# Performance work log

Hardware: AMD Instinct MI355X
Metric: run time of the kernel (lower is better)

## Reference

```python
import jax, jax.numpy as jnp
import numpy as np

N_CHARS = 256
EMB = 1024
HID = 2048
SEQ = 4096


def setup_inputs() -> dict:
    key = jax.random.key(0)
    ks = jax.random.split(key, 12)
    s = 0.02
    return {
        "input_seq": jax.random.randint(ks[0], (SEQ,), 0, N_CHARS),
        "hidden": jnp.zeros((HID,), jnp.float32),
        "cell": jnp.zeros((HID,), jnp.float32),
        "emb": jax.random.normal(ks[1], (N_CHARS, EMB), jnp.float32) * s,
        # gate weights stored as [concat, hidden] so step does z @ W + b
        "Wf": jax.random.normal(ks[2], (EMB + HID, HID), jnp.float32) * s,
        "bf": jnp.zeros((HID,), jnp.float32),
        "Wi": jax.random.normal(ks[3], (EMB + HID, HID), jnp.float32) * s,
        "bi": jnp.zeros((HID,), jnp.float32),
        "Wo": jax.random.normal(ks[4], (EMB + HID, HID), jnp.float32) * s,
        "bo": jnp.zeros((HID,), jnp.float32),
        "Wc": jax.random.normal(ks[5], (EMB + HID, HID), jnp.float32) * s,
        "bc": jnp.zeros((HID,), jnp.float32),
        "Wy": jax.random.normal(ks[6], (HID, N_CHARS), jnp.float32) * s,
        "by": jnp.zeros((N_CHARS,), jnp.float32),
    }


def reference(input_seq, hidden, cell, emb, Wf, bf, Wi, bi, Wo, bo, Wc, bc, Wy, by):
    x = emb[input_seq]  # [S, EMB] embedding lookup for whole sequence

    def step(carry, xt):
        h, c = carry
        z = jnp.concatenate([xt, h])           # [EMB+HID]
        f = jax.nn.sigmoid(z @ Wf + bf)        # forget gate
        i = jax.nn.sigmoid(z @ Wi + bi)        # input gate
        g = jnp.tanh(z @ Wc + bc)              # cell candidate
        o = jax.nn.sigmoid(z @ Wo + bo)        # output gate
        c_new = f * c + i * g
        h_new = o * jnp.tanh(c_new)
        y = h_new @ Wy + by                    # [N_CHARS]
        return (h_new, c_new), y

    (h_fin, c_fin), preds = jax.lax.scan(step, (hidden, cell), x)
    return preds, h_fin, c_fin
```

## Files before the change

kernel.cpp:

```cpp
#include <hip/hip_runtime.h>
#include <hip/hip_bf16.h>
#include <stdint.h>

#define NCH  256
#define EMB  1024
#define HID  2048
#define SEQL 4096

static constexpr size_t EG_OFF   = 0;
static constexpr size_t EG_BYTES = (size_t)NCH * 8192 * 4;
static constexpr size_t HS_OFF   = EG_OFF + EG_BYTES;
static constexpr size_t HS_BYTES = (size_t)SEQL * HID * 4;
static constexpr size_t HB_OFF   = HS_OFF + HS_BYTES;
static constexpr size_t HB_BYTES = 2 * HID * 8;
static constexpr size_t CF_OFF   = HB_OFF + HB_BYTES;
static constexpr size_t CF_BYTES = HID * 4;
static constexpr size_t WS_NEED  = CF_OFF + CF_BYTES;

__global__ __launch_bounds__(256) void eg_gemm(
    const float* __restrict__ emb,
    const float* __restrict__ Wf, const float* __restrict__ bf,
    const float* __restrict__ Wi, const float* __restrict__ bi,
    const float* __restrict__ Wo, const float* __restrict__ bo,
    const float* __restrict__ Wc, const float* __restrict__ bc,
    float* __restrict__ Eg)
{
    const int nb  = blockIdx.x & 63;
    const int cb  = blockIdx.x >> 6;
    const int tid = threadIdx.x;
    const int col = tid & 127;
    const int gate = col >> 5;
    const int jj   = col & 31;
    const int j    = nb * 32 + jj;
    const int mh   = tid >> 7;

    __shared__ float embT[32][65];
    __shared__ float Wt[32][128];

    float acc[32];
#pragma unroll
    for (int m = 0; m < 32; ++m) acc[m] = 0.f;

    for (int k0 = 0; k0 < EMB; k0 += 32) {
        __syncthreads();
        for (int i = tid; i < 64 * 32; i += 256) {
            int c = i >> 5, kk = i & 31;
            embT[kk][c] = emb[(size_t)(cb * 64 + c) * EMB + k0 + kk];
        }
        for (int i = tid; i < 32 * 128; i += 256) {
            int kk = i >> 7, cl = i & 127;
            int g2 = cl >> 5;
            int jx = nb * 32 + (cl & 31);
            const float* Wp = (g2 == 0) ? Wf : (g2 == 1) ? Wi : (g2 == 2) ? Wo : Wc;
            Wt[kk][cl] = Wp[(size_t)(k0 + kk) * HID + jx];
        }
        __syncthreads();
#pragma unroll 8
        for (int kk = 0; kk < 32; ++kk) {
            float w = Wt[kk][col];
#pragma unroll
            for (int m = 0; m < 32; ++m)
                acc[m] += embT[kk][mh * 32 + m] * w;
        }
    }
    const float* bias = (gate == 0) ? bf : (gate == 1) ? bi : (gate == 2) ? bo : bc;
    float bv = bias[j];
    for (int m = 0; m < 32; ++m) {
        int c = cb * 64 + mh * 32 + m;
        Eg[(size_t)c * 8192 + (j >> 3) * 32 + gate * 8 + (j & 7)] = acc[m] + bv;
    }
}

__device__ inline void poll2(const void* p0, const void* p1, uint4& a, uint4& b)
{
    asm volatile(
        "global_load_dwordx4 %0, %2, off sc0 sc1\n\t"
        "global_load_dwordx4 %1, %3, off sc0 sc1\n\t"
        "s_waitcnt vmcnt(0)"
        : "=&v"(a), "=&v"(b)
        : "v"(p0), "v"(p1)
        : "memory");
}

#define REP32(M) M(0) M(1) M(2) M(3) M(4) M(5) M(6) M(7) M(8) M(9) M(10) M(11) \
  M(12) M(13) M(14) M(15) M(16) M(17) M(18) M(19) M(20) M(21) M(22) M(23)      \
  M(24) M(25) M(26) M(27) M(28) M(29) M(30) M(31)

__global__ __launch_bounds__(512, 2) void lstm_seq(
    const int*   __restrict__ seq,
    const float* __restrict__ h0,
    const float* __restrict__ c0,
    const float* __restrict__ Wf, const float* __restrict__ Wi,
    const float* __restrict__ Wo, const float* __restrict__ Wc,
    const float* __restrict__ Eg,
    float* __restrict__ Hs,
    unsigned long long* hb2, float* cfin)
{
    const int cu   = blockIdx.x;
    const int tid  = threadIdx.x;
    const int lane = tid & 63;
    const int wave = tid >> 6;
    const int g    = lane >> 4;
    const int kp   = lane & 15;
    const int jcol = cu * 8 + wave;

    const float* W = (g == 0) ? Wf : (g == 1) ? Wi : (g == 2) ? Wo : Wc;

    const float* Wb = W + (size_t)(1024 + kp * 4) * HID + jcol;
#define WDECL(i) float4 w##i;
    REP32(WDECL)
#undef WDECL
#define WLOAD(i) { w##i.x = Wb[(size_t)((i)*64+0)*HID]; \
                   w##i.y = Wb[(size_t)((i)*64+1)*HID]; \
                   w##i.z = Wb[(size_t)((i)*64+2)*HID]; \
                   w##i.w = Wb[(size_t)((i)*64+3)*HID]; \
                   asm volatile("" : "+a"(w##i.x), "+a"(w##i.y), \
                                     "+a"(w##i.z), "+a"(w##i.w)); }
    REP32(WLOAD)
#undef WLOAD

    __shared__ __align__(16) float h_lds[HID];
    __shared__ int seq_lds[SEQL];

    for (int i = tid; i < SEQL; i += 512) seq_lds[i] = seq[i];
    for (int i = tid; i < HID;  i += 512) h_lds[i]   = h0[i];
    float c = 0.f;
    if (lane == 0) c = c0[jcol];
    __syncthreads();

    const float4* hp = (const float4*)h_lds;

    for (int t = 0; t < SEQL; ++t) {
        float egv = Eg[(size_t)seq_lds[t] * 8192 + cu * 32 + g * 8 + wave];

        float accv[4] = {0.f, 0.f, 0.f, 0.f};
#define WMAC(i) { float4 hv = hp[(i)*16 + kp]; \
                  accv[(i)&3] += w##i.x*hv.x + w##i.y*hv.y + w##i.z*hv.z + w##i.w*hv.w; }
        REP32(WMAC)
#undef WMAC
        float sum = (accv[0] + accv[1]) + (accv[2] + accv[3]);

        sum += __shfl_xor(sum, 1, 16);
        sum += __shfl_xor(sum, 2, 16);
        sum += __shfl_xor(sum, 4, 16);
        sum += __shfl_xor(sum, 8, 16);

        float pre = sum + egv;
        float act;
        if (g < 3) {
            act = 1.f / (1.f + __expf(-pre));
        } else {
            float e = __expf(2.f * pre);
            act = 1.f - 2.f / (e + 1.f);
        }
        float i_ = __shfl(act, 16, 64);
        float o_ = __shfl(act, 32, 64);
        float g_ = __shfl(act, 48, 64);

        if (lane == 0) {
            c = act * c + i_ * g_;
            float e2 = __expf(2.f * c);
            float hn = o_ * (1.f - 2.f / (e2 + 1.f));
            Hs[(size_t)t * HID + jcol] = hn;
            unsigned long long pk =
                ((unsigned long long)(unsigned)(t + 1) << 32) |
                (unsigned long long)__float_as_uint(hn);
            __hip_atomic_store(&hb2[(size_t)((t + 1) & 1) * HID + jcol], pk,
                               __ATOMIC_RELAXED, __HIP_MEMORY_SCOPE_AGENT);
        }

        if (t + 1 < SEQL) {
            const unsigned tgt = (unsigned)(t + 1);
            unsigned long long* sl = hb2 + (size_t)((t + 1) & 1) * HID;
            const void* p0 = (const void*)(sl + 4 * tid);
            const void* p1 = (const void*)(sl + 4 * tid + 2);
            uint4 a, b;
            poll2(p0, p1, a, b);
            while (a.y < tgt || a.w < tgt || b.y < tgt || b.w < tgt) {
                __builtin_amdgcn_s_sleep(1);
                poll2(p0, p1, a, b);
            }
            __syncthreads();
            float4 hv;
            hv.x = __uint_as_float(a.x);
            hv.y = __uint_as_float(a.z);
            hv.z = __uint_as_float(b.x);
            hv.w = __uint_as_float(b.z);
            ((float4*)h_lds)[tid] = hv;
            __syncthreads();
        }
    }

    if (lane == 0) cfin[jcol] = c;
}

__global__ __launch_bounds__(256) void y_gemm(
    const float* __restrict__ Hs, const float* __restrict__ Wy,
    const float* __restrict__ by, float* __restrict__ out)
{
    const int rb  = blockIdx.x * 16;
    const int tid = threadIdx.x;
    __shared__ float A[16][68];
    float acc[16];
#pragma unroll
    for (int r = 0; r < 16; ++r) acc[r] = 0.f;

    for (int k0 = 0; k0 < HID; k0 += 64) {
        __syncthreads();
        for (int i = tid; i < 16 * 64; i += 256) {
            int r = i >> 6, kk = i & 63;
            A[r][kk] = Hs[(size_t)(rb + r) * HID + k0 + kk];
        }
        __syncthreads();
#pragma unroll 8
        for (int kk = 0; kk < 64; ++kk) {
            float b = Wy[(size_t)(k0 + kk) * NCH + tid];
#pragma unroll
            for (int r = 0; r < 16; ++r) acc[r] += A[r][kk] * b;
        }
    }
    float bv = by[tid];
    for (int r = 0; r < 16; ++r)
        out[(size_t)(rb + r) * NCH + tid] = acc[r] + bv;
}

__global__ void fin_copy(const float* __restrict__ Hs,
                         const float* __restrict__ cfin,
                         float* __restrict__ out)
{
    int i = blockIdx.x * 256 + threadIdx.x;
    if (i < HID)
        out[(size_t)SEQL * NCH + i] = Hs[(size_t)(SEQL - 1) * HID + i];
    else
        out[(size_t)SEQL * NCH + i] = cfin[i - HID];
}

extern "C" void kernel_launch(void* const* d_in, const int* in_sizes, int n_in,
                              void* d_out, int out_size, void* d_ws, size_t ws_size,
                              hipStream_t stream)
{
    if (n_in < 14 || ws_size < WS_NEED) return;

    const int*   seq = (const int*)  d_in[0];
    const float* h0  = (const float*)d_in[1];
    const float* c0  = (const float*)d_in[2];
    const float* emb = (const float*)d_in[3];
    const float* Wf  = (const float*)d_in[4];
    const float* bf  = (const float*)d_in[5];
    const float* Wi  = (const float*)d_in[6];
    const float* bi  = (const float*)d_in[7];
    const float* Wo  = (const float*)d_in[8];
    const float* bo  = (const float*)d_in[9];
    const float* Wc  = (const float*)d_in[10];
    const float* bc  = (const float*)d_in[11];
    const float* Wy  = (const float*)d_in[12];
    const float* by  = (const float*)d_in[13];

    char* ws = (char*)d_ws;
    float*              Eg   = (float*)(ws + EG_OFF);
    float*              Hs   = (float*)(ws + HS_OFF);
    unsigned long long* hb2  = (unsigned long long*)(ws + HB_OFF);
    float*              cfin = (float*)(ws + CF_OFF);
    float*              out  = (float*)d_out;

    hipMemsetAsync(hb2, 0, HB_BYTES, stream);

    eg_gemm<<<256, 256, 0, stream>>>(emb, Wf, bf, Wi, bi, Wo, bo, Wc, bc, Eg);

    lstm_seq<<<256, 512, 0, stream>>>(seq, h0, c0, Wf, Wi, Wo, Wc, Eg,
                                      Hs, hb2, cfin);

    y_gemm<<<256, 256, 0, stream>>>(Hs, Wy, by, out);

    fin_copy<<<16, 256, 0, stream>>>(Hs, cfin, out);
}
```

Baseline: 24.88 ms.

## Double-buffer hidden state in LDS and drop one barrier per step

Makes the LDS hidden-state buffer double-buffered by timestep parity, which lets one of the two __syncthreads per recurrence step be removed. Polling now first spins on a single 64-bit atomic load before issuing the bulk dwordx4 loads. The cell update is computed redundantly in every lane, so lane 0 no longer serializes it. The asm constraints that forced weights into AGPRs are also removed, which leaves register placement to the compiler and may change spilling or occupancy.

```diff
diff --git a/kernel.cpp b/kernel.cpp
--- a/kernel.cpp
+++ b/kernel.cpp
@@ -71,7 +71,7 @@
     }
 }
 
-__device__ inline void poll2(const void* p0, const void* p1, uint4& a, uint4& b)
+__device__ inline void bulk2(const void* p0, const void* p1, uint4& a, uint4& b)
 {
     asm volatile(
         "global_load_dwordx4 %0, %2, off sc0 sc1\n\t"
@@ -113,26 +113,22 @@
 #define WLOAD(i) { w##i.x = Wb[(size_t)((i)*64+0)*HID]; \
                    w##i.y = Wb[(size_t)((i)*64+1)*HID]; \
                    w##i.z = Wb[(size_t)((i)*64+2)*HID]; \
-                   w##i.w = Wb[(size_t)((i)*64+3)*HID]; \
-                   asm volatile("" : "+a"(w##i.x), "+a"(w##i.y), \
-                                     "+a"(w##i.z), "+a"(w##i.w)); }
+                   w##i.w = Wb[(size_t)((i)*64+3)*HID]; }
     REP32(WLOAD)
 #undef WLOAD
 
-    __shared__ __align__(16) float h_lds[HID];
+    __shared__ __align__(16) float h_lds[2][HID];
     __shared__ int seq_lds[SEQL];
 
     for (int i = tid; i < SEQL; i += 512) seq_lds[i] = seq[i];
-    for (int i = tid; i < HID;  i += 512) h_lds[i]   = h0[i];
-    float c = 0.f;
-    if (lane == 0) c = c0[jcol];
+    for (int i = tid; i < HID;  i += 512) h_lds[0][i] = h0[i];
+    float c = c0[jcol];
     __syncthreads();
-
-    const float4* hp = (const float4*)h_lds;
 
     for (int t = 0; t < SEQL; ++t) {
         float egv = Eg[(size_t)seq_lds[t] * 8192 + cu * 32 + g * 8 + wave];
 
+        const float4* hp = (const float4*)(h_lds[t & 1]);
         float accv[4] = {0.f, 0.f, 0.f, 0.f};
 #define WMAC(i) { float4 hv = hp[(i)*16 + kp]; \
                   accv[(i)&3] += w##i.x*hv.x + w##i.y*hv.y + w##i.z*hv.z + w##i.w*hv.w; }
@@ -153,14 +149,16 @@
             float e = __expf(2.f * pre);
             act = 1.f - 2.f / (e + 1.f);
         }
+        float f_ = __shfl(act, 0,  64);
         float i_ = __shfl(act, 16, 64);
         float o_ = __shfl(act, 32, 64);
         float g_ = __shfl(act, 48, 64);
 
+        c = f_ * c + i_ * g_;
+        float e2 = __expf(2.f * c);
+        float hn = o_ * (1.f - 2.f / (e2 + 1.f));
+
         if (lane == 0) {
-            c = act * c + i_ * g_;
-            float e2 = __expf(2.f * c);
-            float hn = o_ * (1.f - 2.f / (e2 + 1.f));
             Hs[(size_t)t * HID + jcol] = hn;
             unsigned long long pk =
                 ((unsigned long long)(unsigned)(t + 1) << 32) |
@@ -172,21 +170,29 @@
         if (t + 1 < SEQL) {
             const unsigned tgt = (unsigned)(t + 1);
             unsigned long long* sl = hb2 + (size_t)((t + 1) & 1) * HID;
-            const void* p0 = (const void*)(sl + 4 * tid);
-            const void* p1 = (const void*)(sl + 4 * tid + 2);
+            unsigned long long* mp = sl + 4 * tid;
+
+            if ((unsigned)(__hip_atomic_load(mp, __ATOMIC_RELAXED,
+                                             __HIP_MEMORY_SCOPE_AGENT) >> 32) < tgt) {
+                do {
+                    __builtin_amdgcn_s_sleep(1);
+                } while ((unsigned)(__hip_atomic_load(mp, __ATOMIC_RELAXED,
+                                                      __HIP_MEMORY_SCOPE_AGENT) >> 32) < tgt);
+            }
+
             uint4 a, b;
-            poll2(p0, p1, a, b);
+            bulk2(mp, mp + 2, a, b);
             while (a.y < tgt || a.w < tgt || b.y < tgt || b.w < tgt) {
                 __builtin_amdgcn_s_sleep(1);
-                poll2(p0, p1, a, b);
+                bulk2(mp, mp + 2, a, b);
             }
-            __syncthreads();
+
             float4 hv;
             hv.x = __uint_as_float(a.x);
             hv.y = __uint_as_float(a.z);
             hv.z = __uint_as_float(b.x);
             hv.w = __uint_as_float(b.z);
-            ((float4*)h_lds)[tid] = hv;
+            ((float4*)h_lds[(t + 1) & 1])[tid] = hv;
             __syncthreads();
         }
     }
```

Result: slower. 25.69 ms (+3.3%).
